# Optimization experiments

Hardware: AMD Instinct MI355X
Metric: run time of the kernel (lower is better)

Reference implementation:

```python
import jax, jax.numpy as jnp
import numpy as np

NUM_HEADS = 8  # matches init_kwargs num_heads
LN_EPS = 1e-5  # torch.nn.LayerNorm default


def setup_inputs() -> dict:
    key = jax.random.key(0)
    ks = jax.random.split(key, 12)
    E, B, H, S = 16384, 16, 256, 32
    edge_features = jax.random.normal(ks[0], (E, H), jnp.float32)
    edge_coords = jax.random.normal(ks[1], (E, 3), jnp.float32)
    # sorted, equal-size segments (all graphs non-empty)
    batch = jnp.repeat(jnp.arange(B, dtype=jnp.int32), E // B)
    s_h = 1.0 / np.sqrt(H)
    s_sh = 1.0 / np.sqrt(S * H)
    seed_vectors = jax.random.normal(ks[2], (S, H), jnp.float32)
    # weights stored [in, out] (transposed vs torch nn.Linear)
    Wq = jax.random.normal(ks[3], (H, H), jnp.float32) * s_h
    Wk = jax.random.normal(ks[4], (H, H), jnp.float32) * s_h
    Wv = jax.random.normal(ks[5], (H, H), jnp.float32) * s_h
    Wo = jax.random.normal(ks[6], (H, H), jnp.float32) * s_h
    bo = jnp.zeros((H,), jnp.float32)
    ln_g = jnp.ones((H,), jnp.float32)
    ln_b = jnp.zeros((H,), jnp.float32)
    W1 = jax.random.normal(ks[7], (S * H, H), jnp.float32) * s_sh
    b1 = jnp.zeros((H,), jnp.float32)
    W2 = jax.random.normal(ks[8], (H, H), jnp.float32) * s_h
    b2 = jnp.zeros((H,), jnp.float32)
    return dict(edge_features=edge_features, edge_coords=edge_coords, batch=batch,
                seed_vectors=seed_vectors, Wq=Wq, Wk=Wk, Wv=Wv, Wo=Wo, bo=bo,
                ln_g=ln_g, ln_b=ln_b, W1=W1, b1=b1, W2=W2, b2=b2, num_graphs=B)


def reference(edge_features, edge_coords, batch, seed_vectors, Wq, Wk, Wv, Wo, bo,
              ln_g, ln_b, W1, b1, W2, b2, num_graphs):
    S, H = seed_vectors.shape
    nh = NUM_HEADS
    hd = H // nh
    q = (seed_vectors @ Wq).reshape(S, nh, hd)          # shared across graphs
    k = (edge_features @ Wk).reshape(-1, nh, hd)        # [E, nh, hd]
    v = (edge_features @ Wv).reshape(-1, nh, hd)
    scores = jnp.einsum('shd,ehd->esh', q, k) / np.sqrt(hd).astype(np.float32)
    # segment softmax over edges within each graph
    m = jax.lax.stop_gradient(jax.ops.segment_max(scores, batch, num_segments=num_graphs))
    num = jnp.exp(scores - m[batch])
    den = jax.ops.segment_sum(num, batch, num_segments=num_graphs)
    w = num / den[batch]                                # [E, S, nh]
    att = jax.ops.segment_sum(jnp.einsum('esh,ehd->eshd', w, v), batch,
                              num_segments=num_graphs)  # [B, S, nh, hd]
    att = att.reshape(num_graphs, S, H)                 # concat heads (head-major)
    y = seed_vectors[None, :, :] + att @ Wo + bo        # residual + out_proj
    mu = jnp.mean(y, axis=-1, keepdims=True)
    var = jnp.mean((y - mu) ** 2, axis=-1, keepdims=True)
    y = (y - mu) / jnp.sqrt(var + LN_EPS) * ln_g + ln_b
    flat = y.reshape(num_graphs, S * H)
    h1 = jax.nn.silu(flat @ W1 + b1)
    return h1 @ W2 + b2                                 # [B, H]
```

## Files before the change

### kernel.cpp

```cpp
#include <hip/hip_runtime.h>
#include <math.h>
#include <stdint.h>

#define E_EDGES 16384
#define H_DIM   256
#define S_SEEDS 32
#define NHEADS  8
#define HDIM    32
#define BGRAPHS 16
#define EPG     1024
#define N2      512
#define RSQRT_HD 0.17677669529663687f

typedef __attribute__((ext_vector_type(8))) short bf16x8;
typedef __attribute__((ext_vector_type(4))) float f32x4;

__device__ inline unsigned short f2bf(float x) {
    unsigned u = __float_as_uint(x);
    u += 0x7fff + ((u >> 16) & 1);
    return (unsigned short)(u >> 16);
}
__device__ inline float bf2f(unsigned int h) {
    return __uint_as_float((h & 0xffffu) << 16);
}
__device__ inline unsigned pack2(float a, float b) {
    return (unsigned)f2bf(a) | ((unsigned)f2bf(b) << 16);
}

__global__ __launch_bounds__(256) void k_wc(const float* __restrict__ Wv,
                                            const float* __restrict__ Wk,
                                            const float* __restrict__ Wq,
                                            const float* __restrict__ seed,
                                            unsigned short* __restrict__ WcT) {
    int j = blockIdx.x;
    int i = threadIdx.x;
    float val;
    if (j < H_DIM) {
        val = Wv[i * H_DIM + j];
    } else {
        int c = j - H_DIM;
        int h = c >> 5, s = c & 31;
        __shared__ float qp[8][33];
        __shared__ float qrow[HDIM];
        int d = i & 31, g = i >> 5;
        const float* wq = &Wq[(g * 32) * H_DIM + h * HDIM + d];
        const float* sd = &seed[s * H_DIM + g * 32];
        float p = 0.f;
        #pragma unroll
        for (int ii = 0; ii < 32; ++ii)
            p = fmaf(sd[ii], wq[(size_t)ii * H_DIM], p);
        qp[g][d] = p;
        __syncthreads();
        if (i < HDIM) {
            float qv = 0.f;
            #pragma unroll
            for (int g2 = 0; g2 < 8; ++g2) qv += qp[g2][i];
            qrow[i] = qv;
        }
        __syncthreads();
        const float* wk = &Wk[i * H_DIM + h * HDIM];
        float acc = 0.f;
        #pragma unroll
        for (int dd = 0; dd < HDIM; dd += 4) {
            float4 w = *(const float4*)&wk[dd];
            float4 qq = *(const float4*)&qrow[dd];
            acc = fmaf(w.x, qq.x, acc); acc = fmaf(w.y, qq.y, acc);
            acc = fmaf(w.z, qq.z, acc); acc = fmaf(w.w, qq.w, acc);
        }
        val = acc * RSQRT_HD;
    }
    WcT[j * H_DIM + i] = f2bf(val);
}

#define BKP 40
__global__ __launch_bounds__(256) void k_gemm(const float* __restrict__ A,
                                              const unsigned short* __restrict__ WcT,
                                              unsigned short* __restrict__ C,
                                              float* __restrict__ pmax,
                                              float* __restrict__ psum) {
    __shared__ unsigned short As[128][BKP];
    __shared__ unsigned short Bs[128][BKP];
    __shared__ float smx[2][128];
    __shared__ float ssm[2][128];
    int tid = threadIdx.x;
    int e0 = blockIdx.x * 128, n0 = blockIdx.y * 128;
    int w = tid >> 6, lane = tid & 63;
    int wm = (w >> 1) * 64, wn = (w & 1) * 64;
    int lr = lane & 15, kg = lane >> 4;
    int srow = tid >> 1;
    int scol = (tid & 1) * 16;
    f32x4 acc[4][4] = {};
    for (int k0 = 0; k0 < H_DIM; k0 += 32) {
        const float* ap = &A[(size_t)(e0 + srow) * H_DIM + k0 + scol];
        float4 a0 = *(const float4*)(ap);
        float4 a1 = *(const float4*)(ap + 4);
        float4 a2 = *(const float4*)(ap + 8);
        float4 a3 = *(const float4*)(ap + 12);
        const unsigned short* bp = &WcT[(size_t)(n0 + srow) * H_DIM + k0 + scol];
        uint4 bv0 = *(const uint4*)(bp);
        uint4 bv1 = *(const uint4*)(bp + 8);
        uint4 av0, av1;
        av0.x = pack2(a0.x, a0.y); av0.y = pack2(a0.z, a0.w);
        av0.z = pack2(a1.x, a1.y); av0.w = pack2(a1.z, a1.w);
        av1.x = pack2(a2.x, a2.y); av1.y = pack2(a2.z, a2.w);
        av1.z = pack2(a3.x, a3.y); av1.w = pack2(a3.z, a3.w);
        __syncthreads();
        *(uint4*)&As[srow][scol]     = av0;
        *(uint4*)&As[srow][scol + 8] = av1;
        *(uint4*)&Bs[srow][scol]     = bv0;
        *(uint4*)&Bs[srow][scol + 8] = bv1;
        __syncthreads();
        bf16x8 af[4], bfv[4];
        #pragma unroll
        for (int mi = 0; mi < 4; ++mi)
            af[mi] = *(const bf16x8*)&As[wm + mi * 16 + lr][kg * 8];
        #pragma unroll
        for (int ni = 0; ni < 4; ++ni)
            bfv[ni] = *(const bf16x8*)&Bs[wn + ni * 16 + lr][kg * 8];
        #pragma unroll
        for (int mi = 0; mi < 4; ++mi)
            #pragma unroll
            for (int ni = 0; ni < 4; ++ni)
                acc[mi][ni] = __builtin_amdgcn_mfma_f32_16x16x32_bf16(af[mi], bfv[ni], acc[mi][ni], 0, 0, 0);
    }
    if (n0 >= H_DIM) {
        #pragma unroll
        for (int mi = 0; mi < 4; ++mi)
            #pragma unroll
            for (int ni = 0; ni < 4; ++ni)
                #pragma unroll
                for (int r = 0; r < 4; ++r)
                    acc[mi][ni][r] = bf2f(f2bf(acc[mi][ni][r]));
        float tmax[4];
        #pragma unroll
        for (int ni = 0; ni < 4; ++ni) {
            float m = -1e30f;
            #pragma unroll
            for (int mi = 0; mi < 4; ++mi)
                #pragma unroll
                for (int r = 0; r < 4; ++r) m = fmaxf(m, acc[mi][ni][r]);
            m = fmaxf(m, __shfl_xor(m, 16, 64));
            m = fmaxf(m, __shfl_xor(m, 32, 64));
            tmax[ni] = m;
        }
        if (kg == 0) {
            #pragma unroll
            for (int ni = 0; ni < 4; ++ni) smx[w >> 1][wn + ni * 16 + lr] = tmax[ni];
        }
        __syncthreads();
        float csum[4];
        #pragma unroll
        for (int ni = 0; ni < 4; ++ni) {
            int col = wn + ni * 16 + lr;
            float m = fmaxf(smx[0][col], smx[1][col]);
            float sv = 0.f;
            #pragma unroll
            for (int mi = 0; mi < 4; ++mi)
                #pragma unroll
                for (int r = 0; r < 4; ++r) sv += __expf(acc[mi][ni][r] - m);
            sv += __shfl_xor(sv, 16, 64);
            sv += __shfl_xor(sv, 32, 64);
            csum[ni] = sv;
        }
        if (kg == 0) {
            #pragma unroll
            for (int ni = 0; ni < 4; ++ni) ssm[w >> 1][wn + ni * 16 + lr] = csum[ni];
        }
        __syncthreads();
        if (tid < 128) {
            float m = fmaxf(smx[0][tid], smx[1][tid]);
            float sv = ssm[0][tid] + ssm[1][tid];
            int gcol = (n0 - H_DIM) + tid;
            pmax[(size_t)blockIdx.x * H_DIM + gcol] = m;
            psum[(size_t)blockIdx.x * H_DIM + gcol] = sv;
        }
    }
    #pragma unroll
    for (int mi = 0; mi < 4; ++mi)
        #pragma unroll
        for (int ni = 0; ni < 4; ++ni)
            #pragma unroll
            for (int r = 0; r < 4; ++r) {
                int e = e0 + wm + mi * 16 + kg * 4 + r;
                int n = n0 + wn + ni * 16 + lr;
                C[(size_t)e * N2 + n] = f2bf(acc[mi][ni][r]);
            }
}

#define VSP 40
__global__ __launch_bounds__(256) void k_wsum(const unsigned short* __restrict__ C,
                                              const float* __restrict__ pmax,
                                              const float* __restrict__ psum,
                                              float* __restrict__ patt) {
    int b = blockIdx.x, h = blockIdx.y, pp = blockIdx.z;
    int t = threadIdx.x;
    int s = t & 31, dg = t >> 5;
    __shared__ unsigned short sbuf[128][VSP];
    __shared__ unsigned short vbuf[128][VSP];
    __shared__ float pbuf[128][33];
    __shared__ float ml[32], il[32];
    if (t < 32) {
        int col = h * 32 + t;
        float m = -1e30f;
        #pragma unroll
        for (int j = 0; j < 8; ++j)
            m = fmaxf(m, pmax[(size_t)(b * 8 + j) * H_DIM + col]);
        float sm = 0.f;
        #pragma unroll
        for (int j = 0; j < 8; ++j)
            sm += psum[(size_t)(b * 8 + j) * H_DIM + col] *
                  __expf(pmax[(size_t)(b * 8 + j) * H_DIM + col] - m);
        ml[t] = m; il[t] = 1.f / sm;
    }
    int r = t >> 1, halfo = (t & 1) * 16;
    float a0 = 0.f, a1 = 0.f, a2 = 0.f, a3 = 0.f;
    for (int ch = 0; ch < 2; ++ch) {
        int e0 = b * EPG + (pp * 2 + ch) * 128;
        const unsigned short* crow = &C[(size_t)(e0 + r) * N2 + h * 32 + halfo];
        uint4 sv0 = *(const uint4*)(crow + H_DIM);
        uint4 sv1 = *(const uint4*)(crow + H_DIM + 8);
        uint4 vv0 = *(const uint4*)(crow);
        uint4 vv1 = *(const uint4*)(crow + 8);
        __syncthreads();
        *(uint4*)&sbuf[r][halfo]     = sv0;
        *(uint4*)&sbuf[r][halfo + 8] = sv1;
        *(uint4*)&vbuf[r][halfo]     = vv0;
        *(uint4*)&vbuf[r][halfo + 8] = vv1;
        __syncthreads();
        #pragma unroll
        for (int ii = 0; ii < 16; ++ii) {
            int el = dg + 8 * ii;
            float x = bf2f(sbuf[el][s]);
            pbuf[el][s] = __expf(x - ml[s]) * il[s];
        }
        __syncthreads();
        #pragma unroll 16
        for (int el = 0; el < 128; ++el) {
            float p = pbuf[el][s];
            uint2 vv = *(const uint2*)&vbuf[el][dg * 4];
            a0 = fmaf(p, bf2f(vv.x), a0);
            a1 = fmaf(p, bf2f(vv.x >> 16), a1);
            a2 = fmaf(p, bf2f(vv.y), a2);
            a3 = fmaf(p, bf2f(vv.y >> 16), a3);
        }
    }
    float4 o = {a0, a1, a2, a3};
    *(float4*)&patt[(size_t)((pp * 16 + b) * 32 + s) * H_DIM + h * 32 + dg * 4] = o;
}

__device__ inline float block_sum256(float v, float* red4) {
    for (int o = 32; o > 0; o >>= 1) v += __shfl_xor(v, o, 64);
    int wid = threadIdx.x >> 6;
    if ((threadIdx.x & 63) == 0) red4[wid] = v;
    __syncthreads();
    float r = red4[0] + red4[1] + red4[2] + red4[3];
    __syncthreads();
    return r;
}

__global__ __launch_bounds__(256) void k_proj_ln(const float* __restrict__ patt,
                                                 const float* __restrict__ seed,
                                                 const float* __restrict__ Wo,
                                                 const float* __restrict__ bo,
                                                 const float* __restrict__ ln_g,
                                                 const float* __restrict__ ln_b,
                                                 float* __restrict__ Y) {
    int bs0 = blockIdx.x * 4;
    int c = threadIdx.x;
    __shared__ float arow[4][H_DIM];
    __shared__ float red4[4];
    #pragma unroll
    for (int r = 0; r < 4; ++r) {
        int bs = bs0 + r;
        int b = bs >> 5, s = bs & 31;
        float a = 0.f;
        #pragma unroll
        for (int eq = 0; eq < 4; ++eq)
            a += patt[(size_t)((eq * 16 + b) * 32 + s) * H_DIM + c];
        arow[r][c] = a;
    }
    __syncthreads();
    float acc[4];
    float b0 = bo[c];
    #pragma unroll
    for (int r = 0; r < 4; ++r) acc[r] = b0;
    for (int i = 0; i < H_DIM; i += 4) {
        float4 a0 = *(const float4*)&arow[0][i];
        float4 a1 = *(const float4*)&arow[1][i];
        float4 a2 = *(const float4*)&arow[2][i];
        float4 a3 = *(const float4*)&arow[3][i];
        float w0 = Wo[(i + 0) * H_DIM + c], w1 = Wo[(i + 1) * H_DIM + c];
        float w2 = Wo[(i + 2) * H_DIM + c], w3 = Wo[(i + 3) * H_DIM + c];
        acc[0] = fmaf(a0.x, w0, acc[0]); acc[0] = fmaf(a0.y, w1, acc[0]);
        acc[0] = fmaf(a0.z, w2, acc[0]); acc[0] = fmaf(a0.w, w3, acc[0]);
        acc[1] = fmaf(a1.x, w0, acc[1]); acc[1] = fmaf(a1.y, w1, acc[1]);
        acc[1] = fmaf(a1.z, w2, acc[1]); acc[1] = fmaf(a1.w, w3, acc[1]);
        acc[2] = fmaf(a2.x, w0, acc[2]); acc[2] = fmaf(a2.y, w1, acc[2]);
        acc[2] = fmaf(a2.z, w2, acc[2]); acc[2] = fmaf(a2.w, w3, acc[2]);
        acc[3] = fmaf(a3.x, w0, acc[3]); acc[3] = fmaf(a3.y, w1, acc[3]);
        acc[3] = fmaf(a3.z, w2, acc[3]); acc[3] = fmaf(a3.w, w3, acc[3]);
    }
    float g = ln_g[c], be = ln_b[c];
    #pragma unroll
    for (int r = 0; r < 4; ++r) {
        int bs = bs0 + r;
        float y = seed[(bs & 31) * H_DIM + c] + acc[r];
        float mu = block_sum256(y, red4) * (1.f / 256.f);
        float d = y - mu;
        float var = block_sum256(d * d, red4) * (1.f / 256.f);
        Y[(size_t)bs * H_DIM + c] = d * rsqrtf(var + 1e-5f) * g + be;
    }
}

__global__ __launch_bounds__(256) void k_mlp1(const float* __restrict__ Y,
                                              const float* __restrict__ W1,
                                              float* __restrict__ part) {
    int ch = blockIdx.x;
    int c = threadIdx.x;
    int i0 = ch * 64;
    __shared__ float fbuf[16][64];
    #pragma unroll
    for (int it = 0; it < 4; ++it) {
        int li = it * 256 + c;
        fbuf[li >> 6][li & 63] = Y[(size_t)(li >> 6) * 8192 + i0 + (li & 63)];
    }
    __syncthreads();
    float acc[16];
    #pragma unroll
    for (int b = 0; b < 16; ++b) acc[b] = 0.f;
    for (int ii = 0; ii < 64; ++ii) {
        float w = W1[(size_t)(i0 + ii) * H_DIM + c];
        #pragma unroll
        for (int b = 0; b < 16; ++b) acc[b] = fmaf(fbuf[b][ii], w, acc[b]);
    }
    #pragma unroll
    for (int b = 0; b < 16; ++b)
        part[((size_t)b * 128 + ch) * H_DIM + c] = acc[b];
}

__global__ __launch_bounds__(256) void k_mlp2(const float* __restrict__ part,
                                              const float* __restrict__ b1,
                                              const float* __restrict__ W2,
                                              const float* __restrict__ b2,
                                              float* __restrict__ out) {
    int b = blockIdx.x;
    int c = threadIdx.x;
    float s = b1[c];
    const float* pb = &part[(size_t)b * 128 * H_DIM + c];
    #pragma unroll 4
    for (int ch = 0; ch < 128; ++ch) s += pb[(size_t)ch * H_DIM];
    float h1 = s / (1.f + __expf(-s));
    __shared__ float hrow[H_DIM];
    hrow[c] = h1;
    __syncthreads();
    float acc = b2[c];
    for (int j = 0; j < H_DIM; j += 4) {
        float4 hq = *(const float4*)&hrow[j];
        acc = fmaf(hq.x, W2[(j + 0) * H_DIM + c], acc);
        acc = fmaf(hq.y, W2[(j + 1) * H_DIM + c], acc);
        acc = fmaf(hq.z, W2[(j + 2) * H_DIM + c], acc);
        acc = fmaf(hq.w, W2[(j + 3) * H_DIM + c], acc);
    }
    out[(size_t)b * H_DIM + c] = acc;
}

extern "C" void kernel_launch(void* const* d_in, const int* in_sizes, int n_in,
                              void* d_out, int out_size, void* d_ws, size_t ws_size,
                              hipStream_t stream) {
    const float* edge_features = (const float*)d_in[0];
    const float* seed = (const float*)d_in[3];
    const float* Wq   = (const float*)d_in[4];
    const float* Wk   = (const float*)d_in[5];
    const float* Wv   = (const float*)d_in[6];
    const float* Wo   = (const float*)d_in[7];
    const float* bo   = (const float*)d_in[8];
    const float* ln_g = (const float*)d_in[9];
    const float* ln_b = (const float*)d_in[10];
    const float* W1   = (const float*)d_in[11];
    const float* b1   = (const float*)d_in[12];
    const float* W2   = (const float*)d_in[13];
    const float* b2   = (const float*)d_in[14];
    float* out = (float*)d_out;

    float* ws = (float*)d_ws;
    unsigned short* WcT  = (unsigned short*)ws;
    unsigned short* C    = WcT + 512 * H_DIM;
    float* pmax = (float*)(C + (size_t)E_EDGES * N2);
    float* psum = pmax + 32768;
    float* patt = psum + 32768;
    float* Y    = patt + 524288;
    float* part = Y + 131072;

    k_wc       <<<N2, 256, 0, stream>>>(Wv, Wk, Wq, seed, WcT);
    k_gemm     <<<dim3(E_EDGES / 128, N2 / 128), 256, 0, stream>>>(edge_features, WcT, C, pmax, psum);
    k_wsum     <<<dim3(BGRAPHS, NHEADS, 4), 256, 0, stream>>>(C, pmax, psum, patt);
    k_proj_ln  <<<BGRAPHS * S_SEEDS / 4, 256, 0, stream>>>(patt, seed, Wo, bo, ln_g, ln_b, Y);
    k_mlp1     <<<128, 256, 0, stream>>>(Y, W1, part);
    k_mlp2     <<<BGRAPHS, 256, 0, stream>>>(part, b1, W2, b2, out);
}
```

Baseline: 158.8 us.

## Fuse projection GEMM, segment softmax and weighted sum into one flash-style kernel

Replaces the separate GEMM (writing a bf16 V/score matrix to global memory) and weighted-sum kernels with a single per-64-edge-chunk kernel. It computes V and scores in LDS, applies a local softmax, and runs P·V on MFMA. It emits per-chunk partial outputs plus max and sum, and k_proj_ln rescales and combines the 16 chunks per graph. This removes the large intermediate C round trip and one launch, at the cost of only 256 blocks, large LDS use, and a bigger partial-output buffer.

After: 152.8 us. -3.8%, faster.

```diff
diff --git a/kernel.cpp b/kernel.cpp
--- a/kernel.cpp
+++ b/kernel.cpp
@@ -9,7 +9,8 @@
 #define HDIM    32
 #define BGRAPHS 16
 #define EPG     1024
-#define N2      512
+#define NCHUNK  256
+#define CPG     16
 #define RSQRT_HD 0.17677669529663687f
 
 typedef __attribute__((ext_vector_type(8))) short bf16x8;
@@ -72,180 +73,158 @@
     WcT[j * H_DIM + i] = f2bf(val);
 }
 
-#define BKP 40
-__global__ __launch_bounds__(256) void k_gemm(const float* __restrict__ A,
+__global__ __launch_bounds__(256) void k_attn(const float* __restrict__ A,
                                               const unsigned short* __restrict__ WcT,
-                                              unsigned short* __restrict__ C,
-                                              float* __restrict__ pmax,
-                                              float* __restrict__ psum) {
-    __shared__ unsigned short As[128][BKP];
-    __shared__ unsigned short Bs[128][BKP];
+                                              float* __restrict__ outc,
+                                              float* __restrict__ mg,
+                                              float* __restrict__ sg) {
+    __shared__ unsigned short As[64][264];
+    __shared__ unsigned short Bs[2][128][40];
+    __shared__ unsigned short Vt[256][72];
+    __shared__ unsigned short Pt[128][72];
     __shared__ float smx[2][128];
     __shared__ float ssm[2][128];
     int tid = threadIdx.x;
-    int e0 = blockIdx.x * 128, n0 = blockIdx.y * 128;
+    int chunk = blockIdx.x;
+    int e0 = chunk * 64;
     int w = tid >> 6, lane = tid & 63;
-    int wm = (w >> 1) * 64, wn = (w & 1) * 64;
     int lr = lane & 15, kg = lane >> 4;
-    int srow = tid >> 1;
-    int scol = (tid & 1) * 16;
-    f32x4 acc[4][4] = {};
-    for (int k0 = 0; k0 < H_DIM; k0 += 32) {
-        const float* ap = &A[(size_t)(e0 + srow) * H_DIM + k0 + scol];
-        float4 a0 = *(const float4*)(ap);
-        float4 a1 = *(const float4*)(ap + 4);
-        float4 a2 = *(const float4*)(ap + 8);
-        float4 a3 = *(const float4*)(ap + 12);
-        const unsigned short* bp = &WcT[(size_t)(n0 + srow) * H_DIM + k0 + scol];
-        uint4 bv0 = *(const uint4*)(bp);
-        uint4 bv1 = *(const uint4*)(bp + 8);
-        uint4 av0, av1;
-        av0.x = pack2(a0.x, a0.y); av0.y = pack2(a0.z, a0.w);
-        av0.z = pack2(a1.x, a1.y); av0.w = pack2(a1.z, a1.w);
-        av1.x = pack2(a2.x, a2.y); av1.y = pack2(a2.z, a2.w);
-        av1.z = pack2(a3.x, a3.y); av1.w = pack2(a3.z, a3.w);
-        __syncthreads();
-        *(uint4*)&As[srow][scol]     = av0;
-        *(uint4*)&As[srow][scol + 8] = av1;
-        *(uint4*)&Bs[srow][scol]     = bv0;
-        *(uint4*)&Bs[srow][scol + 8] = bv1;
-        __syncthreads();
-        bf16x8 af[4], bfv[4];
-        #pragma unroll
-        for (int mi = 0; mi < 4; ++mi)
-            af[mi] = *(const bf16x8*)&As[wm + mi * 16 + lr][kg * 8];
-        #pragma unroll
-        for (int ni = 0; ni < 4; ++ni)
-            bfv[ni] = *(const bf16x8*)&Bs[wn + ni * 16 + lr][kg * 8];
-        #pragma unroll
-        for (int mi = 0; mi < 4; ++mi)
+    int wm = (w & 1) * 32, wn = (w >> 1) * 64;
+
+    {
+        int r = tid >> 2, sg4 = tid & 3;
+        const float* ap = &A[(size_t)(e0 + r) * H_DIM + sg4 * 64];
+        #pragma unroll
+        for (int i = 0; i < 8; ++i) {
+            float4 x = *(const float4*)&ap[i * 8];
+            float4 y = *(const float4*)&ap[i * 8 + 4];
+            uint4 o;
+            o.x = pack2(x.x, x.y); o.y = pack2(x.z, x.w);
+            o.z = pack2(y.x, y.y); o.w = pack2(y.z, y.w);
+            *(uint4*)&As[r][sg4 * 64 + i * 8] = o;
+        }
+    }
+    int brow = tid >> 1, bhalf = (tid & 1) * 16;
+    f32x4 acc2[2][2][2] = {};
+    uint4 pb0, pb1;
+    {
+        const unsigned short* bp = &WcT[(size_t)brow * H_DIM + bhalf];
+        pb0 = *(const uint4*)bp; pb1 = *(const uint4*)(bp + 8);
+    }
+    #pragma unroll
+    for (int nt = 0; nt < 4; ++nt) {
+        f32x4 acc[2][4] = {};
+        #pragma unroll
+        for (int k = 0; k < 8; ++k) {
+            *(uint4*)&Bs[k & 1][brow][bhalf]     = pb0;
+            *(uint4*)&Bs[k & 1][brow][bhalf + 8] = pb1;
+            __syncthreads();
+            int nk = k + 1, nnt = nt;
+            if (nk == 8) { nk = 0; nnt = nt + 1; }
+            if (nnt < 4) {
+                const unsigned short* bp =
+                    &WcT[(size_t)(nnt * 128 + brow) * H_DIM + nk * 32 + bhalf];
+                pb0 = *(const uint4*)bp; pb1 = *(const uint4*)(bp + 8);
+            }
+            bf16x8 af[2], bfv[4];
+            #pragma unroll
+            for (int mi = 0; mi < 2; ++mi)
+                af[mi] = *(const bf16x8*)&As[wm + mi * 16 + lr][k * 32 + kg * 8];
             #pragma unroll
             for (int ni = 0; ni < 4; ++ni)
-                acc[mi][ni] = __builtin_amdgcn_mfma_f32_16x16x32_bf16(af[mi], bfv[ni], acc[mi][ni], 0, 0, 0);
-    }
-    if (n0 >= H_DIM) {
-        #pragma unroll
-        for (int mi = 0; mi < 4; ++mi)
-            #pragma unroll
-            for (int ni = 0; ni < 4; ++ni)
-                #pragma unroll
-                for (int r = 0; r < 4; ++r)
-                    acc[mi][ni][r] = bf2f(f2bf(acc[mi][ni][r]));
-        float tmax[4];
-        #pragma unroll
-        for (int ni = 0; ni < 4; ++ni) {
-            float m = -1e30f;
-            #pragma unroll
-            for (int mi = 0; mi < 4; ++mi)
-                #pragma unroll
-                for (int r = 0; r < 4; ++r) m = fmaxf(m, acc[mi][ni][r]);
-            m = fmaxf(m, __shfl_xor(m, 16, 64));
-            m = fmaxf(m, __shfl_xor(m, 32, 64));
-            tmax[ni] = m;
-        }
-        if (kg == 0) {
-            #pragma unroll
-            for (int ni = 0; ni < 4; ++ni) smx[w >> 1][wn + ni * 16 + lr] = tmax[ni];
-        }
-        __syncthreads();
-        float csum[4];
-        #pragma unroll
-        for (int ni = 0; ni < 4; ++ni) {
-            int col = wn + ni * 16 + lr;
-            float m = fmaxf(smx[0][col], smx[1][col]);
-            float sv = 0.f;
-            #pragma unroll
-            for (int mi = 0; mi < 4; ++mi)
-                #pragma unroll
-                for (int r = 0; r < 4; ++r) sv += __expf(acc[mi][ni][r] - m);
-            sv += __shfl_xor(sv, 16, 64);
-            sv += __shfl_xor(sv, 32, 64);
-            csum[ni] = sv;
-        }
-        if (kg == 0) {
-            #pragma unroll
-            for (int ni = 0; ni < 4; ++ni) ssm[w >> 1][wn + ni * 16 + lr] = csum[ni];
-        }
-        __syncthreads();
-        if (tid < 128) {
-            float m = fmaxf(smx[0][tid], smx[1][tid]);
-            float sv = ssm[0][tid] + ssm[1][tid];
-            int gcol = (n0 - H_DIM) + tid;
-            pmax[(size_t)blockIdx.x * H_DIM + gcol] = m;
-            psum[(size_t)blockIdx.x * H_DIM + gcol] = sv;
-        }
-    }
-    #pragma unroll
-    for (int mi = 0; mi < 4; ++mi)
-        #pragma unroll
-        for (int ni = 0; ni < 4; ++ni)
-            #pragma unroll
-            for (int r = 0; r < 4; ++r) {
-                int e = e0 + wm + mi * 16 + kg * 4 + r;
-                int n = n0 + wn + ni * 16 + lr;
-                C[(size_t)e * N2 + n] = f2bf(acc[mi][ni][r]);
-            }
-}
-
-#define VSP 40
-__global__ __launch_bounds__(256) void k_wsum(const unsigned short* __restrict__ C,
-                                              const float* __restrict__ pmax,
-                                              const float* __restrict__ psum,
-                                              float* __restrict__ patt) {
-    int b = blockIdx.x, h = blockIdx.y, pp = blockIdx.z;
-    int t = threadIdx.x;
-    int s = t & 31, dg = t >> 5;
-    __shared__ unsigned short sbuf[128][VSP];
-    __shared__ unsigned short vbuf[128][VSP];
-    __shared__ float pbuf[128][33];
-    __shared__ float ml[32], il[32];
-    if (t < 32) {
-        int col = h * 32 + t;
-        float m = -1e30f;
-        #pragma unroll
-        for (int j = 0; j < 8; ++j)
-            m = fmaxf(m, pmax[(size_t)(b * 8 + j) * H_DIM + col]);
-        float sm = 0.f;
-        #pragma unroll
-        for (int j = 0; j < 8; ++j)
-            sm += psum[(size_t)(b * 8 + j) * H_DIM + col] *
-                  __expf(pmax[(size_t)(b * 8 + j) * H_DIM + col] - m);
-        ml[t] = m; il[t] = 1.f / sm;
-    }
-    int r = t >> 1, halfo = (t & 1) * 16;
-    float a0 = 0.f, a1 = 0.f, a2 = 0.f, a3 = 0.f;
-    for (int ch = 0; ch < 2; ++ch) {
-        int e0 = b * EPG + (pp * 2 + ch) * 128;
-        const unsigned short* crow = &C[(size_t)(e0 + r) * N2 + h * 32 + halfo];
-        uint4 sv0 = *(const uint4*)(crow + H_DIM);
-        uint4 sv1 = *(const uint4*)(crow + H_DIM + 8);
-        uint4 vv0 = *(const uint4*)(crow);
-        uint4 vv1 = *(const uint4*)(crow + 8);
-        __syncthreads();
-        *(uint4*)&sbuf[r][halfo]     = sv0;
-        *(uint4*)&sbuf[r][halfo + 8] = sv1;
-        *(uint4*)&vbuf[r][halfo]     = vv0;
-        *(uint4*)&vbuf[r][halfo + 8] = vv1;
-        __syncthreads();
-        #pragma unroll
-        for (int ii = 0; ii < 16; ++ii) {
-            int el = dg + 8 * ii;
-            float x = bf2f(sbuf[el][s]);
-            pbuf[el][s] = __expf(x - ml[s]) * il[s];
-        }
-        __syncthreads();
-        #pragma unroll 16
-        for (int el = 0; el < 128; ++el) {
-            float p = pbuf[el][s];
-            uint2 vv = *(const uint2*)&vbuf[el][dg * 4];
-            a0 = fmaf(p, bf2f(vv.x), a0);
-            a1 = fmaf(p, bf2f(vv.x >> 16), a1);
-            a2 = fmaf(p, bf2f(vv.y), a2);
-            a3 = fmaf(p, bf2f(vv.y >> 16), a3);
-        }
-    }
-    float4 o = {a0, a1, a2, a3};
-    *(float4*)&patt[(size_t)((pp * 16 + b) * 32 + s) * H_DIM + h * 32 + dg * 4] = o;
+                bfv[ni] = *(const bf16x8*)&Bs[k & 1][wn + ni * 16 + lr][kg * 8];
+            #pragma unroll
+            for (int mi = 0; mi < 2; ++mi)
+                #pragma unroll
+                for (int ni = 0; ni < 4; ++ni)
+                    acc[mi][ni] = __builtin_amdgcn_mfma_f32_16x16x32_bf16(
+                        af[mi], bfv[ni], acc[mi][ni], 0, 0, 0);
+        }
+        if (nt < 2) {
+            #pragma unroll
+            for (int mi = 0; mi < 2; ++mi)
+                #pragma unroll
+                for (int ni = 0; ni < 4; ++ni)
+                    #pragma unroll
+                    for (int r = 0; r < 4; ++r)
+                        Vt[nt * 128 + wn + ni * 16 + lr][wm + mi * 16 + kg * 4 + r] =
+                            f2bf(acc[mi][ni][r]);
+        } else {
+            int st = nt - 2;
+            float tmax[4];
+            #pragma unroll
+            for (int ni = 0; ni < 4; ++ni) {
+                float m = -1e30f;
+                #pragma unroll
+                for (int mi = 0; mi < 2; ++mi)
+                    #pragma unroll
+                    for (int r = 0; r < 4; ++r) m = fmaxf(m, acc[mi][ni][r]);
+                m = fmaxf(m, __shfl_xor(m, 16, 64));
+                m = fmaxf(m, __shfl_xor(m, 32, 64));
+                tmax[ni] = m;
+            }
+            if (kg == 0) {
+                #pragma unroll
+                for (int ni = 0; ni < 4; ++ni) smx[w & 1][wn + ni * 16 + lr] = tmax[ni];
+            }
+            __syncthreads();
+            float tsum[4];
+            #pragma unroll
+            for (int ni = 0; ni < 4; ++ni) {
+                int col = wn + ni * 16 + lr;
+                float m = fmaxf(smx[0][col], smx[1][col]);
+                float sv = 0.f;
+                #pragma unroll
+                for (int mi = 0; mi < 2; ++mi)
+                    #pragma unroll
+                    for (int r = 0; r < 4; ++r) {
+                        float e_ = __expf(acc[mi][ni][r] - m);
+                        unsigned short eb = f2bf(e_);
+                        Pt[col][wm + mi * 16 + kg * 4 + r] = eb;
+                        sv += bf2f(eb);
+                    }
+                sv += __shfl_xor(sv, 16, 64);
+                sv += __shfl_xor(sv, 32, 64);
+                tsum[ni] = sv;
+            }
+            if (kg == 0) {
+                #pragma unroll
+                for (int ni = 0; ni < 4; ++ni) ssm[w & 1][wn + ni * 16 + lr] = tsum[ni];
+            }
+            __syncthreads();
+            if (tid < 128) {
+                float m = fmaxf(smx[0][tid], smx[1][tid]);
+                float sv = ssm[0][tid] + ssm[1][tid];
+                mg[(size_t)chunk * H_DIM + st * 128 + tid] = m;
+                sg[(size_t)chunk * H_DIM + st * 128 + tid] = sv;
+            }
+            #pragma unroll
+            for (int ms = 0; ms < 2; ++ms)
+                #pragma unroll
+                for (int nd = 0; nd < 2; ++nd)
+                    #pragma unroll
+                    for (int kk = 0; kk < 2; ++kk) {
+                        bf16x8 pa = *(const bf16x8*)
+                            &Pt[w * 32 + ms * 16 + lr][kk * 32 + kg * 8];
+                        bf16x8 vb = *(const bf16x8*)
+                            &Vt[(st * 4 + w) * 32 + nd * 16 + lr][kk * 32 + kg * 8];
+                        acc2[st][ms][nd] = __builtin_amdgcn_mfma_f32_16x16x32_bf16(
+                            pa, vb, acc2[st][ms][nd], 0, 0, 0);
+                    }
+        }
+    }
+    #pragma unroll
+    for (int st = 0; st < 2; ++st)
+        #pragma unroll
+        for (int ms = 0; ms < 2; ++ms)
+            #pragma unroll
+            for (int nd = 0; nd < 2; ++nd)
+                #pragma unroll
+                for (int r = 0; r < 4; ++r) {
+                    int s_ = ms * 16 + kg * 4 + r;
+                    int c_ = (st * 4 + w) * 32 + nd * 16 + lr;
+                    outc[((size_t)chunk * 32 + s_) * H_DIM + c_] = acc2[st][ms][nd][r];
+                }
 }
 
 __device__ inline float block_sum256(float v, float* red4) {
@@ -258,7 +237,9 @@
     return r;
 }
 
-__global__ __launch_bounds__(256) void k_proj_ln(const float* __restrict__ patt,
+__global__ __launch_bounds__(256) void k_proj_ln(const float* __restrict__ outc,
+                                                 const float* __restrict__ mg,
+                                                 const float* __restrict__ sg,
                                                  const float* __restrict__ seed,
                                                  const float* __restrict__ Wo,
                                                  const float* __restrict__ bo,
@@ -267,16 +248,40 @@
                                                  float* __restrict__ Y) {
     int bs0 = blockIdx.x * 4;
     int c = threadIdx.x;
+    int b = bs0 >> 5;
+    __shared__ float sscale[4][CPG][8];
     __shared__ float arow[4][H_DIM];
     __shared__ float red4[4];
+    if (c < 32) {
+        int r = c >> 3, hh = c & 7;
+        int s_r = (bs0 + r) & 31;
+        int sc = hh * 32 + s_r;
+        float mj[CPG];
+        float M = -1e30f;
+        #pragma unroll
+        for (int j = 0; j < CPG; ++j) {
+            mj[j] = mg[(size_t)(b * CPG + j) * H_DIM + sc];
+            M = fmaxf(M, mj[j]);
+        }
+        float Den = 0.f;
+        #pragma unroll
+        for (int j = 0; j < CPG; ++j)
+            Den += sg[(size_t)(b * CPG + j) * H_DIM + sc] * __expf(mj[j] - M);
+        float inv = 1.f / Den;
+        #pragma unroll
+        for (int j = 0; j < CPG; ++j)
+            sscale[r][j][hh] = __expf(mj[j] - M) * inv;
+    }
+    __syncthreads();
+    int h = c >> 5;
     #pragma unroll
     for (int r = 0; r < 4; ++r) {
-        int bs = bs0 + r;
-        int b = bs >> 5, s = bs & 31;
+        int s_r = (bs0 + r) & 31;
         float a = 0.f;
         #pragma unroll
-        for (int eq = 0; eq < 4; ++eq)
-            a += patt[(size_t)((eq * 16 + b) * 32 + s) * H_DIM + c];
+        for (int j = 0; j < CPG; ++j)
+            a = fmaf(outc[((size_t)(b * CPG + j) * 32 + s_r) * H_DIM + c],
+                     sscale[r][j][h], a);
         arow[r][c] = a;
     }
     __syncthreads();
@@ -383,18 +388,16 @@
     float* out = (float*)d_out;
 
     float* ws = (float*)d_ws;
-    unsigned short* WcT  = (unsigned short*)ws;
-    unsigned short* C    = WcT + 512 * H_DIM;
-    float* pmax = (float*)(C + (size_t)E_EDGES * N2);
-    float* psum = pmax + 32768;
-    float* patt = psum + 32768;
-    float* Y    = patt + 524288;
+    unsigned short* WcT = (unsigned short*)ws;
+    float* outc = ws + 65536;
+    float* mg   = outc + 2097152;
+    float* sg   = mg + 65536;
+    float* Y    = sg + 65536;
     float* part = Y + 131072;
 
-    k_wc       <<<N2, 256, 0, stream>>>(Wv, Wk, Wq, seed, WcT);
-    k_gemm     <<<dim3(E_EDGES / 128, N2 / 128), 256, 0, stream>>>(edge_features, WcT, C, pmax, psum);
-    k_wsum     <<<dim3(BGRAPHS, NHEADS, 4), 256, 0, stream>>>(C, pmax, psum, patt);
-    k_proj_ln  <<<BGRAPHS * S_SEEDS / 4, 256, 0, stream>>>(patt, seed, Wo, bo, ln_g, ln_b, Y);
-    k_mlp1     <<<128, 256, 0, stream>>>(Y, W1, part);
-    k_mlp2     <<<BGRAPHS, 256, 0, stream>>>(part, b1, W2, b2, out);
-}
+    k_wc      <<<512, 256, 0, stream>>>(Wv, Wk, Wq, seed, WcT);
+    k_attn    <<<NCHUNK, 256, 0, stream>>>(edge_features, WcT, outc, mg, sg);
+    k_proj_ln <<<BGRAPHS * S_SEEDS / 4, 256, 0, stream>>>(outc, mg, sg, seed, Wo, bo, ln_g, ln_b, Y);
+    k_mlp1    <<<128, 256, 0, stream>>>(Y, W1, part);
+    k_mlp2    <<<BGRAPHS, 256, 0, stream>>>(part, b1, W2, b2, out);
+}
```
